# Performance work log

Hardware: AMD Instinct MI355X
Metric: run time of the kernel (lower is better)

The kernel has to match this reference:

```python
import jax, jax.numpy as jnp
import numpy as np

N_ACTIVE = 200000
GRID = 96
C_IN = 128
C_OUT = 128
K = 27  # 3x3x3 kernel offsets
BN_EPS = 1e-4  # scn.BatchNormalization default eps


def _build_rulebook(rng):
    """Sample N_ACTIVE unique voxels in a GRID^3 volume and build the
    submanifold-conv neighbor table: nbr_idx[k, i] = index of the active
    voxel at offset k from voxel i, or -1 if that site is inactive."""
    total = GRID ** 3
    flat = rng.choice(total, size=N_ACTIVE, replace=False).astype(np.int64)
    # flat -> dense lookup of active index
    lut = np.full(total, -1, dtype=np.int32)
    lut[flat] = np.arange(N_ACTIVE, dtype=np.int32)
    z = flat % GRID
    y = (flat // GRID) % GRID
    x = flat // (GRID * GRID)
    offs = np.array([(dx, dy, dz) for dx in (-1, 0, 1)
                     for dy in (-1, 0, 1) for dz in (-1, 0, 1)], dtype=np.int64)
    nbr = np.full((K, N_ACTIVE), -1, dtype=np.int32)
    for k, (dx, dy, dz) in enumerate(offs):
        nx, ny, nz = x + dx, y + dy, z + dz
        ok = ((nx >= 0) & (nx < GRID) & (ny >= 0) & (ny < GRID)
              & (nz >= 0) & (nz < GRID))
        nflat = np.where(ok, nx * GRID * GRID + ny * GRID + nz, 0)
        hit = np.where(ok, lut[nflat], -1)
        nbr[k] = hit
    return nbr


def setup_inputs() -> dict:
    key = jax.random.key(0)
    k1, k2 = jax.random.split(key)
    rng = np.random.default_rng(0)
    nbr_idx = jnp.asarray(_build_rulebook(rng))  # [27, N] int32
    features = jax.random.normal(k1, (N_ACTIVE, C_IN), dtype=jnp.float32)
    # Kaiming-ish scaled conv weights, one [Cin, Cout] matrix per offset
    W = jax.random.normal(k2, (K, C_IN, C_OUT), dtype=jnp.float32) * (
        1.0 / np.sqrt(K * C_IN))
    gamma = jnp.ones((C_OUT,), dtype=jnp.float32)
    beta = jnp.zeros((C_OUT,), dtype=jnp.float32)
    return {"features": features, "nbr_idx": nbr_idx, "W": W,
            "gamma": gamma, "beta": beta}


def reference(features, nbr_idx, W, gamma, beta):
    # --- Submanifold 3x3x3 convolution (gather -> GEMM -> accumulate) ---
    # Output sites == input sites; for each kernel offset k, gather the
    # neighbor's feature row (zero if inactive) and accumulate g @ W[k].
    out = jnp.zeros((features.shape[0], W.shape[-1]), dtype=features.dtype)
    for k in range(K):  # fixed small loop over 27 kernel offsets
        idx = nbr_idx[k]                         # [N]
        valid = (idx >= 0)
        g = features[jnp.maximum(idx, 0)]        # [N, Cin] irregular gather
        g = jnp.where(valid[:, None], g, 0.0)
        out = out + g @ W[k]                     # [N, Cout]
    # --- BatchNormalization over active sites (training batch stats) ---
    mean = jnp.mean(out, axis=0)
    var = jnp.mean(jnp.square(out - mean), axis=0)
    out = (out - mean) * (gamma * jax.lax.rsqrt(var + BN_EPS)) + beta
    # --- ReLU ---
    return jnp.maximum(out, 0.0)
```

## Files before the change

### kernel.cpp

```cpp
#include <hip/hip_runtime.h>
#include <hip/hip_bf16.h>
#include <cstdint>
#include <cstddef>

#define N_ACT 200000
#define CH 128
#define NOFF 27
#define TM 128

typedef __bf16 v8bf __attribute__((ext_vector_type(8)));
typedef float v4f __attribute__((ext_vector_type(4)));

__device__ __forceinline__ unsigned short f2bf(float f) {
    union { float f; unsigned int u; } x; x.f = f;
    unsigned int lsb = (x.u >> 16) & 1u;
    x.u += 0x7fffu + lsb;
    return (unsigned short)(x.u >> 16);
}

__device__ __forceinline__ void gload_lds16(const void* g, void* l) {
    __builtin_amdgcn_global_load_lds(
        (const __attribute__((address_space(1))) unsigned int*)g,
        (__attribute__((address_space(3))) unsigned int*)l,
        16, 0, 0);
}

__global__ void cast_feat(const float* __restrict__ in,
                          unsigned short* __restrict__ out) {
    long long i = (long long)blockIdx.x * blockDim.x + threadIdx.x;
    long long base = i * 8;
    if (base >= (long long)N_ACT * CH) return;
    const float4* p = (const float4*)(in + base);
    float4 a = p[0], b = p[1];
    unsigned int w0 = (unsigned)f2bf(a.x) | ((unsigned)f2bf(a.y) << 16);
    unsigned int w1 = (unsigned)f2bf(a.z) | ((unsigned)f2bf(a.w) << 16);
    unsigned int w2 = (unsigned)f2bf(b.x) | ((unsigned)f2bf(b.y) << 16);
    unsigned int w3 = (unsigned)f2bf(b.z) | ((unsigned)f2bf(b.w) << 16);
    *(uint4*)(out + base) = make_uint4(w0, w1, w2, w3);
}

__global__ void prep_w(const float* __restrict__ W,
                       unsigned short* __restrict__ Wtp,
                       float* __restrict__ stats,
                       float* __restrict__ zpage) {
    int k = blockIdx.x;
    int t = threadIdx.x;
    if (k == 0 && t < 2 * CH) stats[t] = 0.0f;
    if (k == 0 && t < 64) zpage[t] = 0.0f;
    const float* wk = W + (size_t)k * CH * CH;
    for (int g = t; g < 2048; g += 256) {
        int q = g >> 9, r = g & 511;
        int jkk = r >> 6, lane = r & 63;
        int j = jkk >> 2, kk = jkk & 3;
        int lr = lane & 15, quad = lane >> 4;
        int cout = q * 32 + j * 16 + lr;
        int cin0 = kk * 32 + quad * 8;
        unsigned int wbuf[4];
        #pragma unroll
        for (int h = 0; h < 4; ++h) {
            unsigned short lo = f2bf(wk[(size_t)(cin0 + 2*h)     * CH + cout]);
            unsigned short hi = f2bf(wk[(size_t)(cin0 + 2*h + 1) * CH + cout]);
            wbuf[h] = (unsigned)lo | ((unsigned)hi << 16);
        }
        *(uint4*)(Wtp + ((size_t)(k * 4 + q) << 12) + (size_t)(jkk * 64 + lane) * 8)
            = make_uint4(wbuf[0], wbuf[1], wbuf[2], wbuf[3]);
    }
}

__global__ __launch_bounds__(256, 2) void conv_mfma(
        const unsigned short* __restrict__ feat,
        const int* __restrict__ nbr,
        const unsigned short* __restrict__ Wtp,
        const unsigned short* __restrict__ zpage,
        float* __restrict__ out,
        float* __restrict__ stats) {
    __shared__ __bf16 As[2 * TM * CH];
    __shared__ int idxL[NOFF * TM];
    __shared__ float sred[256];

    const int t    = threadIdx.x;
    const int row0 = blockIdx.x * TM;
    const int wid  = t >> 6;
    const int lane = t & 63;
    const int lr   = lane & 15;
    const int quad = lane >> 4;
    const int sc   = lane & 15;
    const int lhi  = lane >> 4;
    const int wv4  = wid * 4;

    for (int e = t; e < NOFF * TM; e += 256) {
        int k = e >> 7, r = e & 127;
        int gr = row0 + r;
        idxL[e] = (gr < N_ACT) ? nbr[(size_t)k * N_ACT + gr] : -1;
    }
    __syncthreads();

    v4f acc[8][2];
    #pragma unroll
    for (int i = 0; i < 8; ++i) {
        acc[i][0] = (v4f){0.f, 0.f, 0.f, 0.f};
        acc[i][1] = (v4f){0.f, 0.f, 0.f, 0.f};
    }

    v8bf B[8];

    auto issueStage = [&](int k, int buf) {
        __bf16* dstbase = As + buf * (TM * CH);
        #pragma unroll
        for (int p = 0; p < 8; ++p) {
            int row = p * 16 + wv4 + lhi;
            int idx = idxL[k * TM + row];
            int gch = (sc - row) & 15;
            const unsigned short* src = (idx >= 0)
                ? feat + ((size_t)idx << 7) + gch * 8
                : zpage + gch * 8;
            gload_lds16(src, dstbase + (size_t)(p * 16 + wv4) * CH);
        }
    };
    auto loadB = [&](int k) {
        const unsigned short* base =
            Wtp + ((size_t)(k * 4 + wid) << 12) + (size_t)lane * 8;
        #pragma unroll
        for (int jkk = 0; jkk < 8; ++jkk)
            B[jkk] = *(const v8bf*)(base + jkk * 512);
    };
    auto mfmaPhase = [&](const __bf16* buf) {
        #pragma unroll
        for (int i = 0; i < 8; ++i) {
            const __bf16* rowp = buf + (i * 16 + lr) * CH;
            v8bf a[4];
            #pragma unroll
            for (int kk = 0; kk < 4; ++kk)
                a[kk] = *(const v8bf*)(rowp + (((kk * 4 + quad + lr) & 15) << 3));
            #pragma unroll
            for (int kk = 0; kk < 4; ++kk) {
                acc[i][0] = __builtin_amdgcn_mfma_f32_16x16x32_bf16(
                    a[kk], B[kk], acc[i][0], 0, 0, 0);
                acc[i][1] = __builtin_amdgcn_mfma_f32_16x16x32_bf16(
                    a[kk], B[4 + kk], acc[i][1], 0, 0, 0);
            }
        }
    };

    issueStage(0, 0);
    loadB(0);
    __syncthreads();

    int cur = 0;
    #pragma unroll 1
    for (int k = 0; k < NOFF; ++k) {
        if (k + 1 < NOFF) issueStage(k + 1, cur ^ 1);
        mfmaPhase(As + cur * (TM * CH));
        if (k + 1 < NOFF) {
            loadB(k + 1);
            __syncthreads();
            cur ^= 1;
        }
    }

    float psum[2] = {0.f, 0.f};
    float psq[2]  = {0.f, 0.f};
    #pragma unroll
    for (int i = 0; i < 8; ++i) {
        #pragma unroll
        for (int r = 0; r < 4; ++r) {
            int grow = row0 + i * 16 + quad * 4 + r;
            if (grow < N_ACT) {
                #pragma unroll
                for (int j = 0; j < 2; ++j) {
                    float v = acc[i][j][r];
                    out[(size_t)grow * CH + wid * 32 + j * 16 + lr] = v;
                    psum[j] += v;
                    psq[j]  += v * v;
                }
            }
        }
    }
    #pragma unroll
    for (int j = 0; j < 2; ++j) {
        psum[j] += __shfl_xor(psum[j], 16, 64);
        psq[j]  += __shfl_xor(psq[j], 16, 64);
        psum[j] += __shfl_xor(psum[j], 32, 64);
        psq[j]  += __shfl_xor(psq[j], 32, 64);
    }
    if (quad == 0) {
        #pragma unroll
        for (int j = 0; j < 2; ++j) {
            int c = wid * 32 + j * 16 + lr;
            sred[c]       = psum[j];
            sred[128 + c] = psq[j];
        }
    }
    __syncthreads();
    if (t < CH) {
        atomicAdd(&stats[t],      sred[t]);
        atomicAdd(&stats[CH + t], sred[128 + t]);
    }
}

__global__ void finalize_stats(const float* __restrict__ gamma,
                               const float* __restrict__ beta,
                               float* __restrict__ stats) {
    int c = threadIdx.x;
    if (c < CH) {
        float inv_n = 1.0f / (float)N_ACT;
        float mean  = stats[c] * inv_n;
        float var   = stats[CH + c] * inv_n - mean * mean;
        float sc    = gamma[c] * rsqrtf(var + 1e-4f);
        stats[2 * CH + c] = sc;
        stats[3 * CH + c] = beta[c] - mean * sc;
    }
}

__global__ void bn_relu(const float* __restrict__ conv,
                        const float* __restrict__ stats,
                        float* __restrict__ out) {
    long long i = (long long)blockIdx.x * blockDim.x + threadIdx.x;
    if (i >= (long long)N_ACT * CH / 4) return;
    int c4 = (int)(i & 31) * 4;
    float4 v  = ((const float4*)conv)[i];
    float4 sc = *(const float4*)(stats + 2 * CH + c4);
    float4 sh = *(const float4*)(stats + 3 * CH + c4);
    float4 o;
    o.x = fmaxf(v.x * sc.x + sh.x, 0.f);
    o.y = fmaxf(v.y * sc.y + sh.y, 0.f);
    o.z = fmaxf(v.z * sc.z + sh.z, 0.f);
    o.w = fmaxf(v.w * sc.w + sh.w, 0.f);
    ((float4*)out)[i] = o;
}

extern "C" void kernel_launch(void* const* d_in, const int* in_sizes, int n_in,
                              void* d_out, int out_size, void* d_ws, size_t ws_size,
                              hipStream_t stream) {
    const float* features = (const float*)d_in[0];
    const int*   nbr      = (const int*)d_in[1];
    const float* W        = (const float*)d_in[2];
    const float* gamma    = (const float*)d_in[3];
    const float* beta     = (const float*)d_in[4];
    float* outp = (float*)d_out;

    char* ws = (char*)d_ws;
    unsigned short* feat_bf = (unsigned short*)ws;
    unsigned short* Wtp     = (unsigned short*)(ws + 51200000);
    float* conv             = (float*)(ws + 51200000 + 884736);
    float* stats            = (float*)(ws + 51200000 + 884736 + 102400000);
    float* zpage            = stats + 4 * CH;

    cast_feat<<<12500, 256, 0, stream>>>(features, feat_bf);
    prep_w<<<NOFF, 256, 0, stream>>>(W, Wtp, stats, zpage);
    conv_mfma<<<(N_ACT + TM - 1) / TM, 256, 0, stream>>>(
        feat_bf, nbr, Wtp, (const unsigned short*)zpage, conv, stats);
    finalize_stats<<<1, CH, 0, stream>>>(gamma, beta, stats);
    bn_relu<<<25000, 256, 0, stream>>>(conv, stats, outp);
}
```

Baseline: 437.2 us.

## Single-buffer conv LDS for higher occupancy, stream indices via DMA, fuse small kernels

```diff
diff --git a/kernel.cpp b/kernel.cpp
--- a/kernel.cpp
+++ b/kernel.cpp
@@ -24,59 +24,69 @@
         (__attribute__((address_space(3))) unsigned int*)l,
         16, 0, 0);
 }
-
-__global__ void cast_feat(const float* __restrict__ in,
-                          unsigned short* __restrict__ out) {
-    long long i = (long long)blockIdx.x * blockDim.x + threadIdx.x;
-    long long base = i * 8;
-    if (base >= (long long)N_ACT * CH) return;
-    const float4* p = (const float4*)(in + base);
-    float4 a = p[0], b = p[1];
-    unsigned int w0 = (unsigned)f2bf(a.x) | ((unsigned)f2bf(a.y) << 16);
-    unsigned int w1 = (unsigned)f2bf(a.z) | ((unsigned)f2bf(a.w) << 16);
-    unsigned int w2 = (unsigned)f2bf(b.x) | ((unsigned)f2bf(b.y) << 16);
-    unsigned int w3 = (unsigned)f2bf(b.z) | ((unsigned)f2bf(b.w) << 16);
-    *(uint4*)(out + base) = make_uint4(w0, w1, w2, w3);
-}
-
-__global__ void prep_w(const float* __restrict__ W,
-                       unsigned short* __restrict__ Wtp,
-                       float* __restrict__ stats,
-                       float* __restrict__ zpage) {
-    int k = blockIdx.x;
+__device__ __forceinline__ void gload_lds4(const void* g, void* l) {
+    __builtin_amdgcn_global_load_lds(
+        (const __attribute__((address_space(1))) unsigned int*)g,
+        (__attribute__((address_space(3))) unsigned int*)l,
+        4, 0, 0);
+}
+
+__global__ void prep_and_cast(const float* __restrict__ features,
+                              const float* __restrict__ W,
+                              unsigned short* __restrict__ feat_bf,
+                              unsigned short* __restrict__ Wtp,
+                              float* __restrict__ stats,
+                              float* __restrict__ zpage) {
     int t = threadIdx.x;
-    if (k == 0 && t < 2 * CH) stats[t] = 0.0f;
-    if (k == 0 && t < 64) zpage[t] = 0.0f;
-    const float* wk = W + (size_t)k * CH * CH;
-    for (int g = t; g < 2048; g += 256) {
-        int q = g >> 9, r = g & 511;
-        int jkk = r >> 6, lane = r & 63;
-        int j = jkk >> 2, kk = jkk & 3;
-        int lr = lane & 15, quad = lane >> 4;
-        int cout = q * 32 + j * 16 + lr;
-        int cin0 = kk * 32 + quad * 8;
-        unsigned int wbuf[4];
-        #pragma unroll
-        for (int h = 0; h < 4; ++h) {
-            unsigned short lo = f2bf(wk[(size_t)(cin0 + 2*h)     * CH + cout]);
-            unsigned short hi = f2bf(wk[(size_t)(cin0 + 2*h + 1) * CH + cout]);
-            wbuf[h] = (unsigned)lo | ((unsigned)hi << 16);
-        }
-        *(uint4*)(Wtp + ((size_t)(k * 4 + q) << 12) + (size_t)(jkk * 64 + lane) * 8)
-            = make_uint4(wbuf[0], wbuf[1], wbuf[2], wbuf[3]);
-    }
-}
-
-__global__ __launch_bounds__(256, 2) void conv_mfma(
+    if (blockIdx.x < NOFF) {
+        int k = blockIdx.x;
+        if (k == 0 && t < 2 * CH) stats[t] = 0.0f;
+        if (k == 0 && t < 64) zpage[t] = 0.0f;
+        const float* wk = W + (size_t)k * CH * CH;
+        for (int g = t; g < 2048; g += 256) {
+            int q = g >> 9, r = g & 511;
+            int jkk = r >> 6, lane = r & 63;
+            int j = jkk >> 2, kk = jkk & 3;
+            int lr = lane & 15, quad = lane >> 4;
+            int cout = q * 32 + j * 16 + lr;
+            int cin0 = kk * 32 + quad * 8;
+            unsigned int wbuf[4];
+            #pragma unroll
+            for (int h = 0; h < 4; ++h) {
+                unsigned short lo = f2bf(wk[(size_t)(cin0 + 2*h)     * CH + cout]);
+                unsigned short hi = f2bf(wk[(size_t)(cin0 + 2*h + 1) * CH + cout]);
+                wbuf[h] = (unsigned)lo | ((unsigned)hi << 16);
+            }
+            *(uint4*)(Wtp + ((size_t)(k * 4 + q) << 12)
+                          + (size_t)(jkk * 64 + lane) * 8)
+                = make_uint4(wbuf[0], wbuf[1], wbuf[2], wbuf[3]);
+        }
+        return;
+    }
+    const long long total = (long long)N_ACT * CH / 8;
+    long long stride = (long long)(gridDim.x - NOFF) * blockDim.x;
+    for (long long i = (long long)(blockIdx.x - NOFF) * blockDim.x + t;
+         i < total; i += stride) {
+        long long base = i * 8;
+        const float4* p = (const float4*)(features + base);
+        float4 a = p[0], b = p[1];
+        unsigned int w0 = (unsigned)f2bf(a.x) | ((unsigned)f2bf(a.y) << 16);
+        unsigned int w1 = (unsigned)f2bf(a.z) | ((unsigned)f2bf(a.w) << 16);
+        unsigned int w2 = (unsigned)f2bf(b.x) | ((unsigned)f2bf(b.y) << 16);
+        unsigned int w3 = (unsigned)f2bf(b.z) | ((unsigned)f2bf(b.w) << 16);
+        *(uint4*)(feat_bf + base) = make_uint4(w0, w1, w2, w3);
+    }
+}
+
+__global__ __launch_bounds__(256, 4) void conv_mfma(
         const unsigned short* __restrict__ feat,
         const int* __restrict__ nbr,
         const unsigned short* __restrict__ Wtp,
         const unsigned short* __restrict__ zpage,
         float* __restrict__ out,
         float* __restrict__ stats) {
-    __shared__ __bf16 As[2 * TM * CH];
-    __shared__ int idxL[NOFF * TM];
-    __shared__ float sred[256];
+    __shared__ __bf16 As[TM * CH];
+    __shared__ int idxS[2][TM];
 
     const int t    = threadIdx.x;
     const int row0 = blockIdx.x * TM;
@@ -88,13 +98,6 @@
     const int lhi  = lane >> 4;
     const int wv4  = wid * 4;
 
-    for (int e = t; e < NOFF * TM; e += 256) {
-        int k = e >> 7, r = e & 127;
-        int gr = row0 + r;
-        idxL[e] = (gr < N_ACT) ? nbr[(size_t)k * N_ACT + gr] : -1;
-    }
-    __syncthreads();
-
     v4f acc[8][2];
     #pragma unroll
     for (int i = 0; i < 8; ++i) {
@@ -104,17 +107,23 @@
 
     v8bf B[8];
 
-    auto issueStage = [&](int k, int buf) {
-        __bf16* dstbase = As + buf * (TM * CH);
+    auto idxDMA = [&](int k, int slot) {
+        const int* src = nbr + (size_t)k * N_ACT;
+        int r0 = min(row0 + lane,      N_ACT - 1);
+        int r1 = min(row0 + 64 + lane, N_ACT - 1);
+        gload_lds4(src + r0, &idxS[slot][0]);
+        gload_lds4(src + r1, &idxS[slot][64]);
+    };
+    auto stageA = [&](int slot) {
         #pragma unroll
         for (int p = 0; p < 8; ++p) {
             int row = p * 16 + wv4 + lhi;
-            int idx = idxL[k * TM + row];
+            int idx = idxS[slot][row];
             int gch = (sc - row) & 15;
             const unsigned short* src = (idx >= 0)
                 ? feat + ((size_t)idx << 7) + gch * 8
                 : zpage + gch * 8;
-            gload_lds16(src, dstbase + (size_t)(p * 16 + wv4) * CH);
+            gload_lds16(src, As + (size_t)(p * 16 + wv4) * CH);
         }
     };
     auto loadB = [&](int k) {
@@ -124,10 +133,10 @@
         for (int jkk = 0; jkk < 8; ++jkk)
             B[jkk] = *(const v8bf*)(base + jkk * 512);
     };
-    auto mfmaPhase = [&](const __bf16* buf) {
+    auto mfmaPhase = [&]() {
         #pragma unroll
         for (int i = 0; i < 8; ++i) {
-            const __bf16* rowp = buf + (i * 16 + lr) * CH;
+            const __bf16* rowp = As + (i * 16 + lr) * CH;
             v8bf a[4];
             #pragma unroll
             for (int kk = 0; kk < 4; ++kk)
@@ -142,19 +151,22 @@
         }
     };
 
-    issueStage(0, 0);
+    if (wid == 0) idxDMA(0, 0);
+    __syncthreads();
+    stageA(0);
+    if (wid == 0) idxDMA(1, 1);
     loadB(0);
     __syncthreads();
 
-    int cur = 0;
     #pragma unroll 1
     for (int k = 0; k < NOFF; ++k) {
-        if (k + 1 < NOFF) issueStage(k + 1, cur ^ 1);
-        mfmaPhase(As + cur * (TM * CH));
+        mfmaPhase();
         if (k + 1 < NOFF) {
+            __syncthreads();
+            stageA((k + 1) & 1);
+            if (wid == 0 && k + 2 < NOFF) idxDMA(k + 2, k & 1);
             loadB(k + 1);
             __syncthreads();
-            cur ^= 1;
         }
     }
 
@@ -187,46 +199,41 @@
         #pragma unroll
         for (int j = 0; j < 2; ++j) {
             int c = wid * 32 + j * 16 + lr;
-            sred[c]       = psum[j];
-            sred[128 + c] = psq[j];
-        }
-    }
-    __syncthreads();
-    if (t < CH) {
-        atomicAdd(&stats[t],      sred[t]);
-        atomicAdd(&stats[CH + t], sred[128 + t]);
-    }
-}
-
-__global__ void finalize_stats(const float* __restrict__ gamma,
-                               const float* __restrict__ beta,
-                               float* __restrict__ stats) {
-    int c = threadIdx.x;
-    if (c < CH) {
-        float inv_n = 1.0f / (float)N_ACT;
-        float mean  = stats[c] * inv_n;
-        float var   = stats[CH + c] * inv_n - mean * mean;
-        float sc    = gamma[c] * rsqrtf(var + 1e-4f);
-        stats[2 * CH + c] = sc;
-        stats[3 * CH + c] = beta[c] - mean * sc;
+            atomicAdd(&stats[c],      psum[j]);
+            atomicAdd(&stats[CH + c], psq[j]);
+        }
     }
 }
 
 __global__ void bn_relu(const float* __restrict__ conv,
                         const float* __restrict__ stats,
+                        const float* __restrict__ gamma,
+                        const float* __restrict__ beta,
                         float* __restrict__ out) {
-    long long i = (long long)blockIdx.x * blockDim.x + threadIdx.x;
-    if (i >= (long long)N_ACT * CH / 4) return;
-    int c4 = (int)(i & 31) * 4;
-    float4 v  = ((const float4*)conv)[i];
-    float4 sc = *(const float4*)(stats + 2 * CH + c4);
-    float4 sh = *(const float4*)(stats + 3 * CH + c4);
-    float4 o;
-    o.x = fmaxf(v.x * sc.x + sh.x, 0.f);
-    o.y = fmaxf(v.y * sc.y + sh.y, 0.f);
-    o.z = fmaxf(v.z * sc.z + sh.z, 0.f);
-    o.w = fmaxf(v.w * sc.w + sh.w, 0.f);
-    ((float4*)out)[i] = o;
+    const long long total = (long long)N_ACT * CH / 4;
+    long long tid = (long long)blockIdx.x * blockDim.x + threadIdx.x;
+    int c4 = (int)(tid & 31) * 4;
+    float sc[4], sh[4];
+    const float inv_n = 1.0f / (float)N_ACT;
+    #pragma unroll
+    for (int j = 0; j < 4; ++j) {
+        int c = c4 + j;
+        float mean = stats[c] * inv_n;
+        float var  = stats[CH + c] * inv_n - mean * mean;
+        float s    = gamma[c] * rsqrtf(var + 1e-4f);
+        sc[j] = s;
+        sh[j] = beta[c] - mean * s;
+    }
+    long long stride = (long long)gridDim.x * blockDim.x;
+    for (long long i = tid; i < total; i += stride) {
+        float4 v = ((const float4*)conv)[i];
+        float4 o;
+        o.x = fmaxf(v.x * sc[0] + sh[0], 0.f);
+        o.y = fmaxf(v.y * sc[1] + sh[1], 0.f);
+        o.z = fmaxf(v.z * sc[2] + sh[2], 0.f);
+        o.w = fmaxf(v.w * sc[3] + sh[3], 0.f);
+        ((float4*)out)[i] = o;
+    }
 }
 
 extern "C" void kernel_launch(void* const* d_in, const int* in_sizes, int n_in,
@@ -246,10 +253,9 @@
     float* stats            = (float*)(ws + 51200000 + 884736 + 102400000);
     float* zpage            = stats + 4 * CH;
 
-    cast_feat<<<12500, 256, 0, stream>>>(features, feat_bf);
-    prep_w<<<NOFF, 256, 0, stream>>>(W, Wtp, stats, zpage);
+    prep_and_cast<<<NOFF + 4096, 256, 0, stream>>>(
+        features, W, feat_bf, Wtp, stats, zpage);
     conv_mfma<<<(N_ACT + TM - 1) / TM, 256, 0, stream>>>(
         feat_bf, nbr, Wtp, (const unsigned short*)zpage, conv, stats);
-    finalize_stats<<<1, CH, 0, stream>>>(gamma, beta, stats);
-    bn_relu<<<25000, 256, 0, stream>>>(conv, stats, outp);
-}
+    bn_relu<<<4096, 256, 0, stream>>>(conv, stats, gamma, beta, outp);
+}
```

After: 385.2 us. 1.14x faster.
